# Kernel optimization log

Measured on AMD Instinct MI355X. Metric: run time of the kernel, lower is better.

The kernel has to match this reference:

```python
import jax, jax.numpy as jnp
import numpy as np

B, T, C = 2, 2048, 2048
N_HEAD, N_KV_HEAD = 16, 4
HEAD_DIM = C // N_HEAD  # 128
N_REP = N_HEAD // N_KV_HEAD  # 4


def setup_inputs() -> dict:
    key = jax.random.key(0)
    ks = jax.random.split(key, 5)
    x = jax.random.normal(ks[0], (B, T, C), dtype=jnp.float32)
    # RoPE freqs (theta=10000), real cos/sin form of torch's complex freqs_cis
    inv_freq = 1.0 / (10000.0 ** (jnp.arange(0, HEAD_DIM, 2, dtype=jnp.float32) / HEAD_DIM))
    angles = jnp.arange(T, dtype=jnp.float32)[:, None] * inv_freq[None, :]  # [T, HEAD_DIM//2]
    freqs_cos = jnp.cos(angles)
    freqs_sin = jnp.sin(angles)
    s = 0.02
    wq = jax.random.normal(ks[1], (C, C), dtype=jnp.float32) * s
    wk = jax.random.normal(ks[2], (N_KV_HEAD * HEAD_DIM, C), dtype=jnp.float32) * s
    wv = jax.random.normal(ks[3], (N_KV_HEAD * HEAD_DIM, C), dtype=jnp.float32) * s
    wo = jax.random.normal(ks[4], (C, C), dtype=jnp.float32) * s
    return {"x": x, "freqs_cos": freqs_cos, "freqs_sin": freqs_sin,
            "wq": wq, "wk": wk, "wv": wv, "wo": wo}


def _apply_rotary(t, cos, sin):
    # t: [B, T, H, D]; pairs (even, odd) treated as complex, multiplied by cos+i*sin
    tr = t.reshape(*t.shape[:-1], -1, 2)  # [B,T,H,D/2,2]
    t0, t1 = tr[..., 0], tr[..., 1]
    c = cos[None, :, None, :]  # [1,T,1,D/2]
    s = sin[None, :, None, :]
    out = jnp.stack([t0 * c - t1 * s, t0 * s + t1 * c], axis=-1)
    return out.reshape(t.shape)


def reference(x, freqs_cos, freqs_sin, wq, wk, wv, wo):
    b, t, _ = x.shape
    xq = (x @ wq.T).reshape(b, t, N_HEAD, HEAD_DIM)
    xk = (x @ wk.T).reshape(b, t, N_KV_HEAD, HEAD_DIM)
    xv = (x @ wv.T).reshape(b, t, N_KV_HEAD, HEAD_DIM)
    xq = _apply_rotary(xq, freqs_cos, freqs_sin)
    xk = _apply_rotary(xk, freqs_cos, freqs_sin)
    # GQA: repeat_interleave kv heads to n_head
    xk_r = jnp.repeat(xk, N_REP, axis=2)
    xv_r = jnp.repeat(xv, N_REP, axis=2)
    # [B,H,T,D]
    q = xq.transpose(0, 2, 1, 3)
    k = xk_r.transpose(0, 2, 1, 3)
    v = xv_r.transpose(0, 2, 1, 3)
    scale = 1.0 / jnp.sqrt(jnp.float32(HEAD_DIM))
    scores = jnp.einsum('bhtd,bhsd->bhts', q, k) * scale
    causal = jnp.tril(jnp.ones((t, t), dtype=bool))
    scores = jnp.where(causal[None, None], scores, jnp.finfo(scores.dtype).min)
    attn = jax.nn.softmax(scores, axis=-1)
    y = jnp.einsum('bhts,bhsd->bhtd', attn, v)
    y = y.transpose(0, 2, 1, 3).reshape(b, t, C)
    return y @ wo.T
```

## Files before the change

### kernel.cpp

```cpp
#include <hip/hip_runtime.h>

typedef __attribute__((ext_vector_type(8))) __bf16 bf16x8;
typedef __attribute__((ext_vector_type(4))) __bf16 bf16x4;
typedef __attribute__((ext_vector_type(4))) float floatx4;

#define MFMA16x16x32 __builtin_amdgcn_mfma_f32_16x16x32_bf16

__device__ __forceinline__ void async_load16(const void* g, void* l) {
  __builtin_amdgcn_global_load_lds((const __attribute__((address_space(1))) void*)g,
                                   (__attribute__((address_space(3))) void*)l, 16, 0, 0);
}

__global__ __launch_bounds__(256) void cast_all_kernel(const float* __restrict__ x,
                                                       const float* __restrict__ wq,
                                                       const float* __restrict__ wk,
                                                       const float* __restrict__ wv,
                                                       const float* __restrict__ wo,
                                                       __bf16* __restrict__ dst) {
  int i = blockIdx.x * blockDim.x + threadIdx.x;
  const float* src;
  int off;
  if (i < 2097152)      { src = x;  off = 0; }
  else if (i < 3145728) { src = wq; off = 2097152; }
  else if (i < 3407872) { src = wk; off = 3145728; }
  else if (i < 3670016) { src = wv; off = 3407872; }
  else                  { src = wo; off = 3670016; }
  float4 v = ((const float4*)src)[i - off];
  bf16x4 o;
  o[0] = (__bf16)v.x; o[1] = (__bf16)v.y; o[2] = (__bf16)v.z; o[3] = (__bf16)v.w;
  *(bf16x4*)(dst + (size_t)i * 4) = o;
}

template <int MODE, int BN>
__global__ __launch_bounds__(512, 1) void gemm_bt(const __bf16* __restrict__ A,
                                                  const __bf16* __restrict__ Bw,
                                                  float* __restrict__ C,
                                                  const float* __restrict__ cs,
                                                  const float* __restrict__ sn,
                                                  __bf16* __restrict__ qb,
                                                  __bf16* __restrict__ kb,
                                                  __bf16* __restrict__ vtg,
                                                  int M, int N, int K) {
  constexpr int NW = BN / 4;
  constexpr int NF = NW / 16;
  constexpr int NBI = BN / 64;
  __shared__ __bf16 As[2][256][64];
  __shared__ __bf16 Bs[2][BN][64];
  const int tid = threadIdx.x;
  const int wave = tid >> 6, lane = tid & 63;
  const int quad = lane >> 4, l16 = lane & 15;
  const int wm2 = wave >> 2, wn4 = wave & 3;
  const int lr = lane >> 3, ls = lane & 7;
  const int segg = ls ^ lr;

  const int nwg = gridDim.x;
  const int wg = (blockIdx.x & 7) * (nwg >> 3) + (blockIdx.x >> 3);
  const int GY = M >> 8;
  const int by = wg % GY, bx = wg / GY;
  const int row0 = by * 256, col0 = bx * BN;

  floatx4 acc[8][NF] = {};
  const __bf16* Ab = A + (size_t)row0 * K + segg * 8;
  const __bf16* Bb = Bw + (size_t)col0 * K + segg * 8;

  auto stage = [&](int sb, int k0) {
#pragma unroll
    for (int i = 0; i < 4; i++)
      async_load16(Ab + (size_t)(wave * 32 + i * 8 + lr) * K + k0,
                   &As[sb][wave * 32 + i * 8][0]);
#pragma unroll
    for (int j = 0; j < NBI; j++)
      async_load16(Bb + (size_t)(wave * (BN / 8) + j * 8 + lr) * K + k0,
                   &Bs[sb][wave * (BN / 8) + j * 8][0]);
  };

  const int NS = K >> 6;
  stage(0, 0);
  stage(1, 64);

#pragma unroll 2
  for (int s = 0; s < NS; s++) {
    const int c = s & 1;
    if (s == NS - 1) {
      asm volatile("s_waitcnt vmcnt(0)" ::: "memory");
    } else if constexpr (NBI == 3) {
      asm volatile("s_waitcnt vmcnt(7)" ::: "memory");
    } else {
      asm volatile("s_waitcnt vmcnt(6)" ::: "memory");
    }
    __builtin_amdgcn_s_barrier();

    bf16x8 af[2][8], bfr[2][NF];
#pragma unroll
    for (int kk = 0; kk < 2; kk++) {
#pragma unroll
      for (int mt = 0; mt < 8; mt++) {
        int row = wm2 * 128 + mt * 16 + l16;
        int seg = (kk * 4 + quad) ^ (row & 7);
        af[kk][mt] = *(const bf16x8*)&As[c][row][seg * 8];
      }
#pragma unroll
      for (int nt = 0; nt < NF; nt++) {
        int row = wn4 * NW + nt * 16 + l16;
        int seg = (kk * 4 + quad) ^ (row & 7);
        bfr[kk][nt] = *(const bf16x8*)&Bs[c][row][seg * 8];
      }
    }
    asm volatile("s_waitcnt lgkmcnt(0)" ::: "memory");
    __builtin_amdgcn_s_barrier();
    if (s + 2 < NS) stage(c, (s + 2) * 64);
    __builtin_amdgcn_s_setprio(1);
#pragma unroll
    for (int kk = 0; kk < 2; kk++)
#pragma unroll
      for (int mt = 0; mt < 8; mt++)
#pragma unroll
        for (int nt = 0; nt < NF; nt++)
          acc[mt][nt] = MFMA16x16x32(af[kk][mt], bfr[kk][nt], acc[mt][nt], 0, 0, 0);
    __builtin_amdgcn_s_setprio(0);
  }

  if (MODE == 0) {
#pragma unroll
    for (int mt = 0; mt < 8; mt++)
#pragma unroll
      for (int nt = 0; nt < NF; nt++)
#pragma unroll
        for (int r = 0; r < 4; r++) {
          int row = row0 + wm2 * 128 + mt * 16 + quad * 4 + r;
          int col = col0 + wn4 * NW + nt * 16 + l16;
          C[(size_t)row * N + col] = acc[mt][nt][r];
        }
  } else {
#pragma unroll
    for (int mt = 0; mt < 8; mt++)
#pragma unroll
      for (int nt = 0; nt < NF; nt++) {
        const int cbase = col0 + wn4 * NW + nt * 16;
        if (cbase < 2560) {
          const int c = cbase + l16;
#pragma unroll
          for (int r = 0; r < 4; r++) {
            int row = row0 + wm2 * 128 + mt * 16 + quad * 4 + r;
            int t = row & 2047;
            float v = acc[mt][nt][r];
            float vp = __shfl_xor(v, 1);
            int i = (c & 127) >> 1;
            float co = cs[t * 64 + i], si = sn[t * 64 + i];
            float rv = v * co + ((c & 1) ? vp : -vp) * si;
            if (cbase < 2048) {
              qb[(size_t)row * 2048 + c] = (__bf16)(rv * 0.1275411391f);
            } else {
              kb[(size_t)row * 512 + c - 2048] = (__bf16)rv;
            }
          }
        }
      }
    __bf16* Vl = &As[0][0][0] + wave * 2048;
    const int brow = row0 + wm2 * 128;
    const int bb = brow >> 11, trow = brow & 2047;
#pragma unroll
    for (int nt = 0; nt < NF; nt++) {
      const int cbase = col0 + wn4 * NW + nt * 16;
      if (cbase >= 2560) {
#pragma unroll
        for (int mt = 0; mt < 8; mt++)
#pragma unroll
          for (int r = 0; r < 4; r++)
            Vl[l16 * 128 + mt * 16 + quad * 4 + r] = (__bf16)acc[mt][nt][r];
        asm volatile("" ::: "memory");
        const int vB = cbase - 2560;
#pragma unroll
        for (int p = 0; p < 4; p++) {
          int vd = p * 4 + (lane >> 4);
          int t0 = (lane & 15) * 8;
          bf16x8 val = *(const bf16x8*)&Vl[vd * 128 + t0];
          *(bf16x8*)&vtg[((size_t)bb * 512 + vB + vd) * 2048 + trow + t0] = val;
        }
        asm volatile("" ::: "memory");
      }
    }
  }
}

__global__ __launch_bounds__(256, 2) void attn_kernel(const __bf16* __restrict__ qb,
                                                      const __bf16* __restrict__ kb,
                                                      const __bf16* __restrict__ vtg,
                                                      __bf16* __restrict__ yb) {
  const int id = blockIdx.x;
  const int q1 = id >> 8;
  const int cc = id & 255;
  const int kvh = cc & 3;
  const int b = (cc >> 2) & 1;
  const int s5 = (cc >> 3) & 31;
  const int tile = q1 ? (63 - s5) : s5;
  const int tid = threadIdx.x, wave = tid >> 6, lane = tid & 63;
  const int h = kvh * 4 + wave;
  const int quad = lane >> 4, l16 = lane & 15;
  const int q0 = tile * 32;
  __shared__ __bf16 Ks[2][64][128];
  __shared__ __bf16 Vt[2][128][64];
  __shared__ __bf16 Ps[4][2][16][64];
  const __bf16* kbase = kb + (size_t)b * 2048 * 512 + kvh * 128;
  const __bf16* vbase = vtg + ((size_t)b * 512 + kvh * 128) * 2048;

  const int u16   = (quad ^ (l16 & 3)) * 16;
  const int b2_64 = (l16 & 4) ? 64 : 0;
  char* const ksb = (char*)Ks;
  char* const vtb = (char*)Vt;
  char* const psb = (char*)Ps + wave * 4096;
  char* const kA0 = ksb + l16 * 256 + u16 + b2_64;
  char* const kB0 = kA0 + 64 - 2 * b2_64;
  char* const kA1 = kA0 + 16384;
  char* const kB1 = kB0 + 16384;
  char* const vA0 = vtb + l16 * 128 + u16 + b2_64;
  char* const vB0 = vA0 + 64 - 2 * b2_64;
  char* const vA1 = vA0 + 16384;
  char* const vB1 = vB0 + 16384;
  char* const prA = psb + l16 * 128 + u16 + b2_64;
  char* const prB = prA + 64 - 2 * b2_64;
  const int h16 = (l16 & 8) ? 16 : 0;
  const int q64 = (quad & 1) * 64;
  char* const pw00 = psb + quad * 512 + (l16 & 7) * 2 + h16 + q64;
  char* const pw10 = psb + quad * 512 + (l16 & 7) * 2 + (16 - h16) + q64;
  char* const pw01 = pw00 + 64 - 2 * q64;
  char* const pw11 = pw10 + 64 - 2 * q64;

  const int klr4 = lane >> 4, kls = lane & 15;
  const int vlr8 = lane >> 3, vls = lane & 7;
  const __bf16* ksrc[4];
  const __bf16* vsrc[4];
#pragma unroll
  for (int i = 0; i < 4; i++) {
    int row = (wave * 4 + i) * 4 + klr4;
    ksrc[i] = kbase + (size_t)row * 512 + (kls ^ (row & 7)) * 8;
    int d = (wave * 4 + i) * 8 + vlr8;
    vsrc[i] = vbase + (size_t)d * 2048 + (vls ^ (d & 7)) * 8;
  }
  char* const kdst = ksb + wave * 4096;
  char* const vdst = vtb + wave * 4096;

  auto stage = [&](int pb, int s0) {
#pragma unroll
    for (int i = 0; i < 4; i++)
      async_load16(ksrc[i] + (size_t)s0 * 512, kdst + pb * 16384 + i * 1024);
#pragma unroll
    for (int i = 0; i < 4; i++)
      async_load16(vsrc[i] + s0, vdst + pb * 16384 + i * 1024);
  };

  bf16x8 qf[2][4];
#pragma unroll
  for (int mt = 0; mt < 2; mt++)
#pragma unroll
    for (int kc = 0; kc < 4; kc++)
      qf[mt][kc] = *(const bf16x8*)(qb + (size_t)(b * 2048 + q0 + mt * 16 + l16) * 2048 +
                                    h * 128 + kc * 32 + quad * 8);
  bf16x8 ones;
#pragma unroll
  for (int j = 0; j < 8; j++) ones[j] = (__bf16)1.0f;
  floatx4 o[2][8] = {};
  floatx4 lsum[2] = {};
  const int nblocks = (tile + 2) >> 1;

  stage(0, 0);

  for (int it = 0; it < nblocks; it++) {
    const int cur = it & 1;
    const int s0 = it * 64;
    asm volatile("s_barrier" ::: "memory");
    if (it + 1 < nblocks) {
      stage(cur ^ 1, s0 + 64);
      asm volatile("s_waitcnt vmcnt(8)" ::: "memory");
    } else {
      asm volatile("s_waitcnt vmcnt(0)" ::: "memory");
    }
    asm volatile("s_barrier" ::: "memory");
    const char* kA = cur ? kA1 : kA0;
    const char* kB = cur ? kB1 : kB0;
    const char* vA = cur ? vA1 : vA0;
    const char* vB = cur ? vB1 : vB0;
    floatx4 sacc[2][4] = {};
    __builtin_amdgcn_s_setprio(1);
#pragma unroll
    for (int kc = 0; kc < 4; kc++) {
      const char* kbp = (kc & 1) ? kB : kA;
      bf16x8 bfr[4];
#pragma unroll
      for (int nt = 0; nt < 4; nt++)
        bfr[nt] = *(const bf16x8*)(kbp + nt * 4096 + (kc >> 1) * 128);
#pragma unroll
      for (int mt = 0; mt < 2; mt++)
#pragma unroll
        for (int nt = 0; nt < 4; nt++)
          sacc[mt][nt] = MFMA16x16x32(qf[mt][kc], bfr[nt], sacc[mt][nt], 0, 0, 0);
    }
    __builtin_amdgcn_s_setprio(0);
    const bool diag = (it == nblocks - 1);
#pragma unroll
    for (int mt = 0; mt < 2; mt++)
#pragma unroll
      for (int r = 0; r < 4; r++) {
        const int qg = q0 + mt * 16 + quad * 4 + r;
#pragma unroll
        for (int nt = 0; nt < 4; nt++) {
          float p = __builtin_exp2f(sacc[mt][nt][r]);
          if (diag) { int keyg = s0 + nt * 16 + l16; p = (keyg <= qg) ? p : 0.f; }
          char* w = (r & 1) ? ((nt < 2) ? pw10 : pw11) : ((nt < 2) ? pw00 : pw01);
          *(__bf16*)(w + mt * 2048 + r * 128 + ((nt & 1) ^ (r >> 1)) * 32) = (__bf16)p;
        }
      }
    __builtin_amdgcn_s_setprio(1);
#pragma unroll
    for (int c2 = 0; c2 < 2; c2++) {
      const char* pr = c2 ? prB : prA;
      const char* vv = c2 ? vB : vA;
      bf16x8 pa[2];
#pragma unroll
      for (int mt = 0; mt < 2; mt++) {
        pa[mt] = *(const bf16x8*)(pr + mt * 2048);
        lsum[mt] = MFMA16x16x32(pa[mt], ones, lsum[mt], 0, 0, 0);
      }
#pragma unroll
      for (int dt = 0; dt < 8; dt++) {
        bf16x8 vf = *(const bf16x8*)(vv + dt * 2048);
#pragma unroll
        for (int mt = 0; mt < 2; mt++)
          o[mt][dt] = MFMA16x16x32(pa[mt], vf, o[mt][dt], 0, 0, 0);
      }
    }
    __builtin_amdgcn_s_setprio(0);
  }
#pragma unroll
  for (int mt = 0; mt < 2; mt++) {
    float inv[4];
#pragma unroll
    for (int r = 0; r < 4; r++) inv[r] = 1.f / lsum[mt][r];
#pragma unroll
    for (int dt = 0; dt < 8; dt++)
#pragma unroll
      for (int r = 0; r < 4; r++) {
        int qg = q0 + mt * 16 + quad * 4 + r;
        yb[(size_t)(b * 2048 + qg) * 2048 + h * 128 + dt * 16 + l16] =
            (__bf16)(o[mt][dt][r] * inv[r]);
      }
  }
}

extern "C" void kernel_launch(void* const* d_in, const int* in_sizes, int n_in,
                              void* d_out, int out_size, void* d_ws, size_t ws_size,
                              hipStream_t stream) {
  const float* x  = (const float*)d_in[0];
  const float* fc = (const float*)d_in[1];
  const float* fs = (const float*)d_in[2];
  const float* wq = (const float*)d_in[3];
  const float* wk = (const float*)d_in[4];
  const float* wv = (const float*)d_in[5];
  const float* wo = (const float*)d_in[6];
  float* out = (float*)d_out;
  char* ws = (char*)d_ws;

  __bf16* xb   = (__bf16*)(ws);
  __bf16* wqkv = (__bf16*)(ws + 16777216);
  __bf16* wob  = (__bf16*)(ws + 29360128);
  __bf16* qbuf = (__bf16*)(ws + 37748736);
  __bf16* kbuf = (__bf16*)(ws + 54525952);
  __bf16* vtg  = (__bf16*)(ws + 58720256);
  __bf16* ybuf = (__bf16*)(ws + 62914560);

  cast_all_kernel<<<18432, 256, 0, stream>>>(x, wq, wk, wv, wo, xb);

  gemm_bt<1, 192><<<256, 512, 0, stream>>>(xb, wqkv, nullptr, fc, fs,
                                           qbuf, kbuf, vtg, 4096, 3072, 2048);

  attn_kernel<<<512, 256, 0, stream>>>(qbuf, kbuf, vtg, ybuf);

  gemm_bt<0, 128><<<256, 512, 0, stream>>>(ybuf, wob, out, nullptr, nullptr,
                                           nullptr, nullptr, nullptr, 4096, 2048, 2048);
}
```

Measured before the change: 304.3 us.

## Restructure GEMM main loop into ping-pong interleaved LDS reads and MFMA phases

Replaces the two-stage prefetch (stage s+2 after reading LDS) with a one-ahead prefetch issued right after the barrier, and splits each k-step into four sub-phases, each loading a quarter of the A fragments and then running its MFMAs. Barriers between the sub-phases make waves alternate between LDS reads and matrix math, in a ping-pong style. The goal is lower register pressure and better overlap of LDS and MFMA work. In exchange, global prefetch depth drops to one tile with a full vmcnt(0) wait each iteration, and the extra barriers per k-step could expose load latency.

```diff
diff --git a/kernel.cpp b/kernel.cpp
--- a/kernel.cpp
+++ b/kernel.cpp
@@ -76,48 +76,47 @@
 
   const int NS = K >> 6;
   stage(0, 0);
-  stage(1, 64);
 
 #pragma unroll 2
-  for (int s = 0; s < NS; s++) {
-    const int c = s & 1;
-    if (s == NS - 1) {
-      asm volatile("s_waitcnt vmcnt(0)" ::: "memory");
-    } else if constexpr (NBI == 3) {
-      asm volatile("s_waitcnt vmcnt(7)" ::: "memory");
-    } else {
-      asm volatile("s_waitcnt vmcnt(6)" ::: "memory");
-    }
-    __builtin_amdgcn_s_barrier();
-
-    bf16x8 af[2][8], bfr[2][NF];
+  for (int t = 0; t < NS; t++) {
+    const int c = t & 1;
+    asm volatile("s_waitcnt vmcnt(0)" ::: "memory");
+    asm volatile("s_barrier" ::: "memory");
+    if (t + 1 < NS) stage(c ^ 1, (t + 1) * 64);
+    bf16x8 bfr[2][NF];
 #pragma unroll
     for (int kk = 0; kk < 2; kk++) {
 #pragma unroll
-      for (int mt = 0; mt < 8; mt++) {
-        int row = wm2 * 128 + mt * 16 + l16;
-        int seg = (kk * 4 + quad) ^ (row & 7);
-        af[kk][mt] = *(const bf16x8*)&As[c][row][seg * 8];
-      }
-#pragma unroll
-      for (int nt = 0; nt < NF; nt++) {
-        int row = wn4 * NW + nt * 16 + l16;
-        int seg = (kk * 4 + quad) ^ (row & 7);
-        bfr[kk][nt] = *(const bf16x8*)&Bs[c][row][seg * 8];
-      }
-    }
-    asm volatile("s_waitcnt lgkmcnt(0)" ::: "memory");
-    __builtin_amdgcn_s_barrier();
-    if (s + 2 < NS) stage(c, (s + 2) * 64);
-    __builtin_amdgcn_s_setprio(1);
-#pragma unroll
-    for (int kk = 0; kk < 2; kk++)
-#pragma unroll
-      for (int mt = 0; mt < 8; mt++)
-#pragma unroll
-        for (int nt = 0; nt < NF; nt++)
-          acc[mt][nt] = MFMA16x16x32(af[kk][mt], bfr[kk][nt], acc[mt][nt], 0, 0, 0);
-    __builtin_amdgcn_s_setprio(0);
+      for (int mh = 0; mh < 2; mh++) {
+        bf16x8 af[4];
+        if (mh == 0) {
+#pragma unroll
+          for (int nt = 0; nt < NF; nt++) {
+            int row = wn4 * NW + nt * 16 + l16;
+            int seg = (kk * 4 + quad) ^ (row & 7);
+            bfr[kk][nt] = *(const bf16x8*)&Bs[c][row][seg * 8];
+          }
+        }
+#pragma unroll
+        for (int mi = 0; mi < 4; mi++) {
+          int row = wm2 * 128 + (mh * 4 + mi) * 16 + l16;
+          int seg = (kk * 4 + quad) ^ (row & 7);
+          af[mi] = *(const bf16x8*)&As[c][row][seg * 8];
+        }
+        asm volatile("s_barrier" ::: "memory");
+        asm volatile("s_waitcnt lgkmcnt(0)" ::: "memory");
+        __builtin_amdgcn_sched_barrier(0);
+        __builtin_amdgcn_s_setprio(1);
+#pragma unroll
+        for (int mi = 0; mi < 4; mi++)
+#pragma unroll
+          for (int nt = 0; nt < NF; nt++)
+            acc[mh * 4 + mi][nt] =
+                MFMA16x16x32(af[mi], bfr[kk][nt], acc[mh * 4 + mi][nt], 0, 0, 0);
+        __builtin_amdgcn_s_setprio(0);
+        asm volatile("s_barrier" ::: "memory");
+      }
+    }
   }
 
   if (MODE == 0) {
```

New measurement: 337.7 us. 1.11x slower.

## Split attention key range across wave pairs and merge partial outputs in LDS

Applied to the files above, without the earlier changes.

The attention kernel now launches twice as many blocks. Each block handles two heads of a KV group, and its waves are split into two key-chunk halves that process the causal key range in parallel with 32-key tiles. The two partial outputs and row sums are combined through shared memory at the end, which is valid because the softmax uses no max subtraction. V is now loaded through registers and written to LDS instead of async copies. The change is meant to improve load balance and occupancy, at the cost of an extra reduction step, more barriers and padded work when the chunk lengths are uneven.

```diff
diff --git a/kernel.cpp b/kernel.cpp
--- a/kernel.cpp
+++ b/kernel.cpp
@@ -188,66 +188,54 @@
                                                       const __bf16* __restrict__ vtg,
                                                       __bf16* __restrict__ yb) {
   const int id = blockIdx.x;
-  const int q1 = id >> 8;
-  const int cc = id & 255;
-  const int kvh = cc & 3;
-  const int b = (cc >> 2) & 1;
-  const int s5 = (cc >> 3) & 31;
-  const int tile = q1 ? (63 - s5) : s5;
+  const int kvh = id & 3, b = (id >> 2) & 1;
+  const int pair = (id >> 3) & 1;
+  const int tile = 63 - (id >> 4);
   const int tid = threadIdx.x, wave = tid >> 6, lane = tid & 63;
-  const int h = kvh * 4 + wave;
+  const int ck = wave >> 1, hw = wave & 1;
+  const int h = kvh * 4 + pair * 2 + hw;
   const int quad = lane >> 4, l16 = lane & 15;
   const int q0 = tile * 32;
+  const int nkb = tile + 1;
+  const int c0 = nkb >> 1;
+  const int L1 = nkb - c0;
+
   __shared__ __bf16 Ks[2][64][128];
   __shared__ __bf16 Vt[2][128][64];
-  __shared__ __bf16 Ps[4][2][16][64];
+  __shared__ __bf16 Ps[4][2][16][32];
+
   const __bf16* kbase = kb + (size_t)b * 2048 * 512 + kvh * 128;
   const __bf16* vbase = vtg + ((size_t)b * 512 + kvh * 128) * 2048;
 
-  const int u16   = (quad ^ (l16 & 3)) * 16;
+  const int klr4 = lane >> 4, kls = lane & 15;
+  const __bf16* ksrc[4];
+  char* kdst[4];
+#pragma unroll
+  for (int j = 0; j < 4; j++) {
+    int lrow = hw * 16 + j * 4 + klr4;
+    ksrc[j] = kbase + (size_t)lrow * 512 + (kls ^ (lrow & 7)) * 8;
+    kdst[j] = (char*)Ks + (ck * 32 + hw * 16 + j * 4) * 256;
+  }
+  const int vdl = lane >> 2, vks = lane & 3;
+  const __bf16* vsrc[4];
+  char* vdst[4];
+#pragma unroll
+  for (int j = 0; j < 4; j++) {
+    int d = hw * 64 + j * 16 + vdl;
+    vsrc[j] = vbase + (size_t)d * 2048 + vks * 8;
+    vdst[j] = (char*)Vt + d * 128 + (((ck * 4 + vks) ^ (d & 7)) * 16);
+  }
+
+  const int u16 = (quad ^ (l16 & 3)) * 16;
   const int b2_64 = (l16 & 4) ? 64 : 0;
-  char* const ksb = (char*)Ks;
-  char* const vtb = (char*)Vt;
-  char* const psb = (char*)Ps + wave * 4096;
-  char* const kA0 = ksb + l16 * 256 + u16 + b2_64;
+  char* const kA0 = (char*)Ks + (ck * 32 + l16) * 256 + u16 + b2_64;
   char* const kB0 = kA0 + 64 - 2 * b2_64;
-  char* const kA1 = kA0 + 16384;
-  char* const kB1 = kB0 + 16384;
-  char* const vA0 = vtb + l16 * 128 + u16 + b2_64;
-  char* const vB0 = vA0 + 64 - 2 * b2_64;
-  char* const vA1 = vA0 + 16384;
-  char* const vB1 = vB0 + 16384;
-  char* const prA = psb + l16 * 128 + u16 + b2_64;
-  char* const prB = prA + 64 - 2 * b2_64;
-  const int h16 = (l16 & 8) ? 16 : 0;
-  const int q64 = (quad & 1) * 64;
-  char* const pw00 = psb + quad * 512 + (l16 & 7) * 2 + h16 + q64;
-  char* const pw10 = psb + quad * 512 + (l16 & 7) * 2 + (16 - h16) + q64;
-  char* const pw01 = pw00 + 64 - 2 * q64;
-  char* const pw11 = pw10 + 64 - 2 * q64;
-
-  const int klr4 = lane >> 4, kls = lane & 15;
-  const int vlr8 = lane >> 3, vls = lane & 7;
-  const __bf16* ksrc[4];
-  const __bf16* vsrc[4];
-#pragma unroll
-  for (int i = 0; i < 4; i++) {
-    int row = (wave * 4 + i) * 4 + klr4;
-    ksrc[i] = kbase + (size_t)row * 512 + (kls ^ (row & 7)) * 8;
-    int d = (wave * 4 + i) * 8 + vlr8;
-    vsrc[i] = vbase + (size_t)d * 2048 + (vls ^ (d & 7)) * 8;
-  }
-  char* const kdst = ksb + wave * 4096;
-  char* const vdst = vtb + wave * 4096;
-
-  auto stage = [&](int pb, int s0) {
-#pragma unroll
-    for (int i = 0; i < 4; i++)
-      async_load16(ksrc[i] + (size_t)s0 * 512, kdst + pb * 16384 + i * 1024);
-#pragma unroll
-    for (int i = 0; i < 4; i++)
-      async_load16(vsrc[i] + s0, vdst + pb * 16384 + i * 1024);
-  };
+  char* const vrd0 = (char*)Vt + l16 * 128 + u16 + (((ck ^ (l16 >> 2)) & 1) ? 64 : 0);
+  char* const psb = (char*)Ps + wave * 2048;
+  char* const prd = psb + l16 * 64 + u16;
+  const int h3 = (l16 >> 3) & 1;
+  char* const pwE = psb + quad * 256 + (l16 & 7) * 2 + h3 * 16;
+  char* const pwO = psb + quad * 256 + (l16 & 7) * 2 + 16 - h3 * 16;
 
   bf16x8 qf[2][4];
 #pragma unroll
@@ -261,89 +249,132 @@
   for (int j = 0; j < 8; j++) ones[j] = (__bf16)1.0f;
   floatx4 o[2][8] = {};
   floatx4 lsum[2] = {};
-  const int nblocks = (tile + 2) >> 1;
-
-  stage(0, 0);
-
-  for (int it = 0; it < nblocks; it++) {
+
+  {
+    const int g0 = ck ? c0 : 0;
+#pragma unroll
+    for (int j = 0; j < 4; j++)
+      async_load16(ksrc[j] + (size_t)g0 * 32 * 512, kdst[j]);
+    bf16x8 vr[4];
+#pragma unroll
+    for (int j = 0; j < 4; j++) vr[j] = *(const bf16x8*)(vsrc[j] + g0 * 32);
+#pragma unroll
+    for (int j = 0; j < 4; j++) *(bf16x8*)(vdst[j]) = vr[j];
+  }
+
+  for (int it = 0; it < L1; it++) {
     const int cur = it & 1;
-    const int s0 = it * 64;
+    const int bc = cur << 14, bn = (cur ^ 1) << 14;
+    asm volatile("s_waitcnt lgkmcnt(0)" ::: "memory");
     asm volatile("s_barrier" ::: "memory");
-    if (it + 1 < nblocks) {
-      stage(cur ^ 1, s0 + 64);
-      asm volatile("s_waitcnt vmcnt(8)" ::: "memory");
+    const bool pf = (it + 1 < L1);
+    int gn = 0;
+    if (pf) {
+      gn = ck ? (c0 + it + 1) : min(it + 1, c0 > 0 ? c0 - 1 : 0);
+#pragma unroll
+      for (int j = 0; j < 4; j++)
+        async_load16(ksrc[j] + (size_t)gn * 32 * 512, kdst[j] + bn);
+      asm volatile("s_waitcnt vmcnt(4)" ::: "memory");
     } else {
       asm volatile("s_waitcnt vmcnt(0)" ::: "memory");
     }
     asm volatile("s_barrier" ::: "memory");
-    const char* kA = cur ? kA1 : kA0;
-    const char* kB = cur ? kB1 : kB0;
-    const char* vA = cur ? vA1 : vA0;
-    const char* vB = cur ? vB1 : vB0;
-    floatx4 sacc[2][4] = {};
+
+    floatx4 sacc[2][2] = {};
     __builtin_amdgcn_s_setprio(1);
 #pragma unroll
     for (int kc = 0; kc < 4; kc++) {
-      const char* kbp = (kc & 1) ? kB : kA;
-      bf16x8 bfr[4];
-#pragma unroll
-      for (int nt = 0; nt < 4; nt++)
-        bfr[nt] = *(const bf16x8*)(kbp + nt * 4096 + (kc >> 1) * 128);
-#pragma unroll
-      for (int mt = 0; mt < 2; mt++)
-#pragma unroll
-        for (int nt = 0; nt < 4; nt++)
-          sacc[mt][nt] = MFMA16x16x32(qf[mt][kc], bfr[nt], sacc[mt][nt], 0, 0, 0);
+      const char* kp = ((kc & 1) ? kB0 : kA0) + bc + (kc >> 1) * 128;
+      bf16x8 bf0 = *(const bf16x8*)(kp);
+      bf16x8 bf1 = *(const bf16x8*)(kp + 4096);
+#pragma unroll
+      for (int mt = 0; mt < 2; mt++) {
+        sacc[mt][0] = MFMA16x16x32(qf[mt][kc], bf0, sacc[mt][0], 0, 0, 0);
+        sacc[mt][1] = MFMA16x16x32(qf[mt][kc], bf1, sacc[mt][1], 0, 0, 0);
+      }
     }
     __builtin_amdgcn_s_setprio(0);
-    const bool diag = (it == nblocks - 1);
+
+    bf16x8 vr[4];
+    if (pf) {
+#pragma unroll
+      for (int j = 0; j < 4; j++) vr[j] = *(const bf16x8*)(vsrc[j] + gn * 32);
+    }
+
+    const int gq = ck ? (c0 + it) : it;
+    const bool diag = (ck == 1) && (it == L1 - 1);
+    const bool inval = (ck == 0) && (it >= c0);
 #pragma unroll
     for (int mt = 0; mt < 2; mt++)
 #pragma unroll
       for (int r = 0; r < 4; r++) {
         const int qg = q0 + mt * 16 + quad * 4 + r;
 #pragma unroll
-        for (int nt = 0; nt < 4; nt++) {
+        for (int nt = 0; nt < 2; nt++) {
           float p = __builtin_exp2f(sacc[mt][nt][r]);
-          if (diag) { int keyg = s0 + nt * 16 + l16; p = (keyg <= qg) ? p : 0.f; }
-          char* w = (r & 1) ? ((nt < 2) ? pw10 : pw11) : ((nt < 2) ? pw00 : pw01);
-          *(__bf16*)(w + mt * 2048 + r * 128 + ((nt & 1) ^ (r >> 1)) * 32) = (__bf16)p;
+          if (diag) { int keyg = gq * 32 + nt * 16 + l16; p = (keyg <= qg) ? p : 0.f; }
+          if (inval) p = 0.f;
+          char* w = (r & 1) ? pwO : pwE;
+          *(__bf16*)(w + mt * 1024 + r * 64 + ((nt ^ ((r >> 1) & 1)) & 1) * 32) =
+              (__bf16)p;
         }
       }
+
     __builtin_amdgcn_s_setprio(1);
-#pragma unroll
-    for (int c2 = 0; c2 < 2; c2++) {
-      const char* pr = c2 ? prB : prA;
-      const char* vv = c2 ? vB : vA;
-      bf16x8 pa[2];
+    bf16x8 pa[2];
+#pragma unroll
+    for (int mt = 0; mt < 2; mt++) {
+      pa[mt] = *(const bf16x8*)(prd + mt * 1024);
+      lsum[mt] = MFMA16x16x32(pa[mt], ones, lsum[mt], 0, 0, 0);
+    }
+#pragma unroll
+    for (int dt = 0; dt < 8; dt++) {
+      bf16x8 vf = *(const bf16x8*)(vrd0 + bc + dt * 2048);
+      o[0][dt] = MFMA16x16x32(pa[0], vf, o[0][dt], 0, 0, 0);
+      o[1][dt] = MFMA16x16x32(pa[1], vf, o[1][dt], 0, 0, 0);
+    }
+    __builtin_amdgcn_s_setprio(0);
+
+    if (pf) {
+#pragma unroll
+      for (int j = 0; j < 4; j++) *(bf16x8*)(vdst[j] + bn) = vr[j];
+    }
+  }
+
+  asm volatile("s_barrier" ::: "memory");
+  {
+    char* mo = (char*)Ks + hw * 16384;
+    char* ml = (char*)Vt + hw * 2048;
+    if (ck == 1) {
 #pragma unroll
       for (int mt = 0; mt < 2; mt++) {
-        pa[mt] = *(const bf16x8*)(pr + mt * 2048);
-        lsum[mt] = MFMA16x16x32(pa[mt], ones, lsum[mt], 0, 0, 0);
-      }
-#pragma unroll
-      for (int dt = 0; dt < 8; dt++) {
-        bf16x8 vf = *(const bf16x8*)(vv + dt * 2048);
-#pragma unroll
-        for (int mt = 0; mt < 2; mt++)
-          o[mt][dt] = MFMA16x16x32(pa[mt], vf, o[mt][dt], 0, 0, 0);
-      }
-    }
-    __builtin_amdgcn_s_setprio(0);
-  }
-#pragma unroll
-  for (int mt = 0; mt < 2; mt++) {
-    float inv[4];
-#pragma unroll
-    for (int r = 0; r < 4; r++) inv[r] = 1.f / lsum[mt][r];
-#pragma unroll
-    for (int dt = 0; dt < 8; dt++)
-#pragma unroll
-      for (int r = 0; r < 4; r++) {
-        int qg = q0 + mt * 16 + quad * 4 + r;
-        yb[(size_t)(b * 2048 + qg) * 2048 + h * 128 + dt * 16 + l16] =
-            (__bf16)(o[mt][dt][r] * inv[r]);
-      }
+#pragma unroll
+        for (int dt = 0; dt < 8; dt++)
+          *(floatx4*)(mo + ((mt * 8 + dt) * 64 + lane) * 16) = o[mt][dt];
+        *(floatx4*)(ml + (mt * 64 + lane) * 16) = lsum[mt];
+      }
+    }
+    asm volatile("s_waitcnt lgkmcnt(0)" ::: "memory");
+    asm volatile("s_barrier" ::: "memory");
+    if (ck == 0) {
+#pragma unroll
+      for (int mt = 0; mt < 2; mt++) {
+        lsum[mt] += *(const floatx4*)(ml + (mt * 64 + lane) * 16);
+        float inv[4];
+#pragma unroll
+        for (int r = 0; r < 4; r++) inv[r] = 1.f / lsum[mt][r];
+#pragma unroll
+        for (int dt = 0; dt < 8; dt++) {
+          floatx4 op = *(const floatx4*)(mo + ((mt * 8 + dt) * 64 + lane) * 16);
+#pragma unroll
+          for (int r = 0; r < 4; r++) {
+            int qg = q0 + mt * 16 + quad * 4 + r;
+            yb[(size_t)(b * 2048 + qg) * 2048 + h * 128 + dt * 16 + l16] =
+                (__bf16)((o[mt][dt][r] + op[r]) * inv[r]);
+          }
+        }
+      }
+    }
   }
 }
 
@@ -373,7 +404,7 @@
   gemm_bt<1, 192><<<256, 512, 0, stream>>>(xb, wqkv, nullptr, fc, fs,
                                            qbuf, kbuf, vtg, 4096, 3072, 2048);
 
-  attn_kernel<<<512, 256, 0, stream>>>(qbuf, kbuf, vtg, ybuf);
+  attn_kernel<<<1024, 256, 0, stream>>>(qbuf, kbuf, vtg, ybuf);
 
   gemm_bt<0, 128><<<256, 512, 0, stream>>>(ybuf, wob, out, nullptr, nullptr,
                                            nullptr, nullptr, nullptr, 4096, 2048, 2048);
```

New measurement: 303.2 us. About the same (-0.4%).
